# Performance work log

Hardware: AMD Instinct MI355X
Metric: run time of the kernel (lower is better)

Reference implementation:

```python
import jax, jax.numpy as jnp
import numpy as np

OUT, IN, R = 4096, 4096, 64
B, S = 4, 4096


def setup_inputs() -> dict:
    key = jax.random.key(0)
    ks = jax.random.split(key, 12)
    return {
        "x": jax.random.normal(ks[0], (B, S, IN), dtype=jnp.float32),
        "W": jax.random.normal(ks[1], (OUT, IN), dtype=jnp.float32) * 0.02,
        "bias": jax.random.normal(ks[2], (OUT,), dtype=jnp.float32) * 0.02,
        "U_top": jax.random.normal(ks[3], (OUT, R), dtype=jnp.float32) / np.sqrt(OUT),
        "S_top": jax.random.uniform(ks[4], (R,), dtype=jnp.float32),
        "Vh_top": jax.random.normal(ks[5], (R, IN), dtype=jnp.float32) / np.sqrt(IN),
        "U_tail": jax.random.normal(ks[6], (OUT, R), dtype=jnp.float32) / np.sqrt(OUT),
        "S_tail": jax.random.uniform(ks[7], (R,), dtype=jnp.float32),
        "Vh_tail": jax.random.normal(ks[8], (R, IN), dtype=jnp.float32) / np.sqrt(IN),
        "alpha": jax.random.normal(ks[9], (R,), dtype=jnp.float32) * 0.01,
        "beta": jax.random.normal(ks[10], (R,), dtype=jnp.float32) * 0.01,
        "R": jax.random.normal(ks[11], (R, R), dtype=jnp.float32) * 0.01,
    }


def reference(x, W, bias, U_top, S_top, Vh_top, U_tail, S_tail, Vh_tail, alpha, beta, R):
    # SALT top: gated singular-value correction, relu(S*alpha + beta)
    sigma_top = jax.nn.relu(S_top * alpha + beta)                    # [r]
    W_top_delta = (U_top * sigma_top[None, :]) @ Vh_top              # [out, in]
    # EDoRA tail: B R A with B = U_tail diag(S_tail), A = Vh_tail
    Bm = U_tail * S_tail[None, :]                                    # [out, r]
    delta_tail = Bm @ (R @ Vh_tail)                                  # [out, in]
    W_tilde = W + W_top_delta + delta_tail
    # F.linear: x @ W_tilde.T + bias
    return jnp.einsum('bsi,oi->bso', x, W_tilde) + bias
```

## Files before the change

kernel.cpp:

```cpp
#include <hip/hip_runtime.h>
#include <hip/hip_bf16.h>

#define OUT_DIM 4096
#define IN_DIM  4096
#define RANK    64
#define M_DIM   16384

typedef short  s16x8 __attribute__((ext_vector_type(8)));
typedef __bf16 b16x8 __attribute__((ext_vector_type(8)));
typedef float  f32x4 __attribute__((ext_vector_type(4)));

template <typename T>
__device__ static inline auto mfma_sel(T a, T b, f32x4 c, int)
    -> decltype(__builtin_amdgcn_mfma_f32_16x16x32_bf16(a, b, c, 0, 0, 0)) {
  return __builtin_amdgcn_mfma_f32_16x16x32_bf16(a, b, c, 0, 0, 0);
}
template <typename T>
__device__ static inline f32x4 mfma_sel(T a, T b, f32x4 c, long) {
  return __builtin_amdgcn_mfma_f32_16x16x32_bf16(
      __builtin_bit_cast(b16x8, a), __builtin_bit_cast(b16x8, b), c, 0, 0, 0);
}
__device__ static inline f32x4 mfma_bf16(s16x8 a, s16x8 b, f32x4 c) {
  return mfma_sel(a, b, c, 0);
}

__device__ static inline unsigned short f2bf(float f) {
  unsigned int u = __float_as_uint(f);
  u += 0x7fffu + ((u >> 16) & 1u);
  return (unsigned short)(u >> 16);
}

__device__ static inline void gload16(const unsigned short* g, unsigned short* l) {
  __builtin_amdgcn_global_load_lds(
      (const __attribute__((address_space(1))) void*)g,
      (__attribute__((address_space(3))) void*)l, 16, 0, 0);
}

__global__ void prep_kernel(const float* __restrict__ U_top, const float* __restrict__ S_top,
                            const float* __restrict__ alpha, const float* __restrict__ beta,
                            const float* __restrict__ U_tail, const float* __restrict__ S_tail,
                            float* __restrict__ A1, float* __restrict__ A2) {
  int idx = blockIdx.x * 256 + threadIdx.x;
  int r = idx & (RANK - 1);
  float sig = S_top[r] * alpha[r] + beta[r];
  sig = sig > 0.f ? sig : 0.f;
  A1[idx] = U_top[idx] * sig;
  A2[idx] = U_tail[idx] * S_tail[r];
}

__global__ void rv_kernel(const float* __restrict__ Rm, const float* __restrict__ Vh_tail,
                          float* __restrict__ RV) {
  const int i  = blockIdx.x * 256 + threadIdx.x;
  const int r0 = blockIdx.y * 8;
  float acc[8] = {};
  for (int q = 0; q < RANK; ++q) {
    float v = Vh_tail[(size_t)q * IN_DIM + i];
#pragma unroll
    for (int rr = 0; rr < 8; ++rr)
      acc[rr] = fmaf(Rm[(r0 + rr) * RANK + q], v, acc[rr]);
  }
#pragma unroll
  for (int rr = 0; rr < 8; ++rr) RV[(size_t)(r0 + rr) * IN_DIM + i] = acc[rr];
}

__global__ void cvt_kernel(const float* __restrict__ x, unsigned short* __restrict__ xb) {
  const long long n8 = (long long)M_DIM * IN_DIM / 8;
  long long idx = (long long)blockIdx.x * blockDim.x + threadIdx.x;
  const long long stride = (long long)gridDim.x * blockDim.x;
  for (; idx < n8; idx += stride) {
    const f32x4* p = (const f32x4*)(x + idx * 8);
    f32x4 v0 = p[0], v1 = p[1];
    s16x8 o;
    o[0] = (short)f2bf(v0[0]); o[1] = (short)f2bf(v0[1]);
    o[2] = (short)f2bf(v0[2]); o[3] = (short)f2bf(v0[3]);
    o[4] = (short)f2bf(v1[0]); o[5] = (short)f2bf(v1[1]);
    o[6] = (short)f2bf(v1[2]); o[7] = (short)f2bf(v1[3]);
    *(s16x8*)(xb + idx * 8) = o;
  }
}

#define WT_O 16
__global__ void wtilde_kernel(const float* __restrict__ W,  const float* __restrict__ A1,
                              const float* __restrict__ A2, const float* __restrict__ Vh_top,
                              const float* __restrict__ RV, unsigned short* __restrict__ Wb) {
  const int i  = blockIdx.x * 256 + threadIdx.x;
  const int o0 = blockIdx.y * WT_O;
  float acc[WT_O];
#pragma unroll
  for (int o = 0; o < WT_O; ++o) acc[o] = W[(size_t)(o0 + o) * IN_DIM + i];
#pragma unroll 4
  for (int r = 0; r < RANK; ++r) {
    float vt = Vh_top[(size_t)r * IN_DIM + i];
    float rv = RV[(size_t)r * IN_DIM + i];
#pragma unroll
    for (int o = 0; o < WT_O; ++o) {
      acc[o] = fmaf(A1[(o0 + o) * RANK + r], vt, acc[o]);
      acc[o] = fmaf(A2[(o0 + o) * RANK + r], rv, acc[o]);
    }
  }
#pragma unroll
  for (int o = 0; o < WT_O; ++o)
    Wb[(size_t)(o0 + o) * IN_DIM + i] = f2bf(acc[o]);
}

#define BM 256
#define BN 256
#define BK 64
#define NT (IN_DIM / BK)

__global__ __launch_bounds__(512, 2) void gemm_kernel(
    const unsigned short* __restrict__ A,
    const unsigned short* __restrict__ Bw,
    const float* __restrict__ bias,
    float* __restrict__ C) {
  __shared__ unsigned short lds[2][2][BM * BK];

  const int tid = threadIdx.x;
  const int l   = tid & 63;
  const int wid = tid >> 6;
  const int wr  = wid >> 2;
  const int wc  = wid & 3;

  const int bid = blockIdx.x;
  const int swz = (bid & 7) * 128 + (bid >> 3);
  const int nt_ = swz >> 6;
  const int mt_ = swz & 63;
  const long long tileM = (long long)mt_ * BM;
  const long long tileN = (long long)nt_ * BN;

  const int rbase = tid >> 3;
  const int c8    = (((tid & 7) ^ (rbase & 7)) << 3);
  const unsigned short* gA = A  + (tileM + rbase) * (long long)IN_DIM + c8;
  const unsigned short* gB = Bw + (tileN + rbase) * (long long)IN_DIM + c8;

  const int kgrp = l >> 4;
  const int x7   = l & 7;
  const int sc0  = (((0 * 4 + kgrp) ^ x7) << 3);
  const int sc1  = (((1 * 4 + kgrp) ^ x7) << 3);
  const int rba  = (wr * 128 + (l & 15)) * BK;
  const int rbb  = (wc * 64  + (l & 15)) * BK;

  f32x4 acc[8][4] = {};

  {
    unsigned short* la = &lds[0][0][tid * 8];
    unsigned short* lb = &lds[0][1][tid * 8];
#pragma unroll
    for (int j = 0; j < 4; ++j) {
      gload16(gA + (long long)j * 64 * IN_DIM, la + j * 4096);
      gload16(gB + (long long)j * 64 * IN_DIM, lb + j * 4096);
    }
    asm volatile("s_waitcnt vmcnt(0)" ::: "memory");
    asm volatile("s_barrier" ::: "memory");
  }

  int buf = 0;
  for (int t = 0; t < NT; ++t) {
    const long long ktn = (long long)(t + 1) * BK;
    const bool more = (t + 1 < NT);
    const unsigned short* lA = lds[buf][0];
    const unsigned short* lB = lds[buf][1];
    unsigned short* la1 = &lds[buf ^ 1][0][tid * 8];
    unsigned short* lb1 = &lds[buf ^ 1][1][tid * 8];

    s16x8 bfr[4][2];
#pragma unroll
    for (int q = 0; q < 4; ++q) {
      if (q == 0) {
#pragma unroll
        for (int n = 0; n < 4; ++n) {
          bfr[n][0] = *(const s16x8*)&lB[rbb + n * 16 * BK + sc0];
          bfr[n][1] = *(const s16x8*)&lB[rbb + n * 16 * BK + sc1];
        }
      }
      s16x8 afr[2][2];
#pragma unroll
      for (int m2 = 0; m2 < 2; ++m2) {
        afr[m2][0] = *(const s16x8*)&lA[rba + (q * 32 + m2 * 16) * BK + sc0];
        afr[m2][1] = *(const s16x8*)&lA[rba + (q * 32 + m2 * 16) * BK + sc1];
      }

      if (more) {
        if (q == 0) {
          gload16(gA + ktn, la1);
          gload16(gA + ktn + 2LL * 64 * IN_DIM, la1 + 2 * 4096);
        } else if (q == 1) {
          gload16(gA + ktn + 1LL * 64 * IN_DIM, la1 + 1 * 4096);
          gload16(gA + ktn + 3LL * 64 * IN_DIM, la1 + 3 * 4096);
        } else if (q == 2) {
          gload16(gB + ktn, lb1);
          gload16(gB + ktn + 1LL * 64 * IN_DIM, lb1 + 4096);
        } else {
          gload16(gB + ktn + 2LL * 64 * IN_DIM, lb1 + 2 * 4096);
          gload16(gB + ktn + 3LL * 64 * IN_DIM, lb1 + 3 * 4096);
        }
      }

      asm volatile("s_barrier" ::: "memory");

      __builtin_amdgcn_s_setprio(1);
#pragma unroll
      for (int m2 = 0; m2 < 2; ++m2)
#pragma unroll
        for (int n = 0; n < 4; ++n)
#pragma unroll
          for (int kk = 0; kk < 2; ++kk)
            acc[q * 2 + m2][n] = mfma_bf16(afr[m2][kk], bfr[n][kk], acc[q * 2 + m2][n]);
      __builtin_amdgcn_s_setprio(0);

      if (q == 3 && more) {
        asm volatile("s_waitcnt vmcnt(0)" ::: "memory");
      }
      asm volatile("s_barrier" ::: "memory");
    }
    buf ^= 1;
  }

  float bv[4];
#pragma unroll
  for (int n = 0; n < 4; ++n) bv[n] = bias[tileN + wc * 64 + n * 16 + (l & 15)];
#pragma unroll
  for (int m = 0; m < 8; ++m) {
    const long long rbase_c = tileM + wr * 128 + m * 16 + (l >> 4) * 4;
#pragma unroll
    for (int r = 0; r < 4; ++r) {
      float* crow = C + (size_t)(rbase_c + r) * OUT_DIM + tileN + wc * 64 + (l & 15);
#pragma unroll
      for (int n = 0; n < 4; ++n) crow[n * 16] = acc[m][n][r] + bv[n];
    }
  }
}

extern "C" void kernel_launch(void* const* d_in, const int* in_sizes, int n_in,
                              void* d_out, int out_size, void* d_ws, size_t ws_size,
                              hipStream_t stream) {
  const float* x       = (const float*)d_in[0];
  const float* W       = (const float*)d_in[1];
  const float* bias    = (const float*)d_in[2];
  const float* U_top   = (const float*)d_in[3];
  const float* S_top   = (const float*)d_in[4];
  const float* Vh_top  = (const float*)d_in[5];
  const float* U_tail  = (const float*)d_in[6];
  const float* S_tail  = (const float*)d_in[7];
  const float* Vh_tail = (const float*)d_in[8];
  const float* alpha   = (const float*)d_in[9];
  const float* beta    = (const float*)d_in[10];
  const float* Rm      = (const float*)d_in[11];

  char* ws = (char*)d_ws;
  unsigned short* xb = (unsigned short*)ws;
  unsigned short* Wb = (unsigned short*)(ws + (size_t)134217728);
  float* A1 = (float*)(ws + (size_t)134217728 + 33554432);
  float* A2 = A1 + (size_t)OUT_DIM * RANK;
  float* RV = A2 + (size_t)OUT_DIM * RANK;

  prep_kernel<<<(OUT_DIM * RANK) / 256, 256, 0, stream>>>(U_top, S_top, alpha, beta,
                                                          U_tail, S_tail, A1, A2);
  rv_kernel<<<dim3(IN_DIM / 256, RANK / 8), 256, 0, stream>>>(Rm, Vh_tail, RV);
  cvt_kernel<<<2048, 256, 0, stream>>>(x, xb);
  wtilde_kernel<<<dim3(IN_DIM / 256, OUT_DIM / WT_O), 256, 0, stream>>>(W, A1, A2,
                                                                        Vh_top, RV, Wb);
  gemm_kernel<<<(M_DIM / BM) * (OUT_DIM / BN), 512, 0, stream>>>(xb, Wb, bias,
                                                                 (float*)d_out);
}
```

Before: 761.1 us.

## Switch GEMM to 32x32x16 MFMA, relax load waits, fold prep kernel away

The main GEMM moves from 16x16x32 to 32x32x16 bf16 MFMA tiles. This reduces the number of LDS fragment reads and MFMA issues per tile and changes the accumulator and epilogue layout. The next-tile prefetch order is swapped to load B first. Partial vmcnt waits replace the full drain, so the wait on global-to-LDS loads overlaps more with compute. Separately, the prep kernel is removed by folding the sigma and S_tail scaling into the rv and wtilde kernels, which saves one launch and its intermediate buffers. The partial vmcnt counts must exactly match the outstanding loads, or the kernel could read stale LDS data.

```diff
diff --git a/kernel.cpp b/kernel.cpp
--- a/kernel.cpp
+++ b/kernel.cpp
@@ -6,22 +6,23 @@
 #define RANK    64
 #define M_DIM   16384
 
-typedef short  s16x8 __attribute__((ext_vector_type(8)));
-typedef __bf16 b16x8 __attribute__((ext_vector_type(8)));
-typedef float  f32x4 __attribute__((ext_vector_type(4)));
+typedef short  s16x8  __attribute__((ext_vector_type(8)));
+typedef __bf16 b16x8  __attribute__((ext_vector_type(8)));
+typedef float  f32x4  __attribute__((ext_vector_type(4)));
+typedef float  f32x16 __attribute__((ext_vector_type(16)));
 
 template <typename T>
-__device__ static inline auto mfma_sel(T a, T b, f32x4 c, int)
-    -> decltype(__builtin_amdgcn_mfma_f32_16x16x32_bf16(a, b, c, 0, 0, 0)) {
-  return __builtin_amdgcn_mfma_f32_16x16x32_bf16(a, b, c, 0, 0, 0);
+__device__ static inline auto mfma32_sel(T a, T b, f32x16 c, int)
+    -> decltype(__builtin_amdgcn_mfma_f32_32x32x16_bf16(a, b, c, 0, 0, 0)) {
+  return __builtin_amdgcn_mfma_f32_32x32x16_bf16(a, b, c, 0, 0, 0);
 }
 template <typename T>
-__device__ static inline f32x4 mfma_sel(T a, T b, f32x4 c, long) {
-  return __builtin_amdgcn_mfma_f32_16x16x32_bf16(
+__device__ static inline f32x16 mfma32_sel(T a, T b, f32x16 c, long) {
+  return __builtin_amdgcn_mfma_f32_32x32x16_bf16(
       __builtin_bit_cast(b16x8, a), __builtin_bit_cast(b16x8, b), c, 0, 0, 0);
 }
-__device__ static inline f32x4 mfma_bf16(s16x8 a, s16x8 b, f32x4 c) {
-  return mfma_sel(a, b, c, 0);
+__device__ static inline f32x16 mfma32(s16x8 a, s16x8 b, f32x16 c) {
+  return mfma32_sel(a, b, c, 0);
 }
 
 __device__ static inline unsigned short f2bf(float f) {
@@ -36,20 +37,8 @@
       (__attribute__((address_space(3))) void*)l, 16, 0, 0);
 }
 
-__global__ void prep_kernel(const float* __restrict__ U_top, const float* __restrict__ S_top,
-                            const float* __restrict__ alpha, const float* __restrict__ beta,
-                            const float* __restrict__ U_tail, const float* __restrict__ S_tail,
-                            float* __restrict__ A1, float* __restrict__ A2) {
-  int idx = blockIdx.x * 256 + threadIdx.x;
-  int r = idx & (RANK - 1);
-  float sig = S_top[r] * alpha[r] + beta[r];
-  sig = sig > 0.f ? sig : 0.f;
-  A1[idx] = U_top[idx] * sig;
-  A2[idx] = U_tail[idx] * S_tail[r];
-}
-
-__global__ void rv_kernel(const float* __restrict__ Rm, const float* __restrict__ Vh_tail,
-                          float* __restrict__ RV) {
+__global__ void rv2_kernel(const float* __restrict__ Rm, const float* __restrict__ Vh_tail,
+                           const float* __restrict__ S_tail, float* __restrict__ RV2) {
   const int i  = blockIdx.x * 256 + threadIdx.x;
   const int r0 = blockIdx.y * 8;
   float acc[8] = {};
@@ -60,7 +49,8 @@
       acc[rr] = fmaf(Rm[(r0 + rr) * RANK + q], v, acc[rr]);
   }
 #pragma unroll
-  for (int rr = 0; rr < 8; ++rr) RV[(size_t)(r0 + rr) * IN_DIM + i] = acc[rr];
+  for (int rr = 0; rr < 8; ++rr)
+    RV2[(size_t)(r0 + rr) * IN_DIM + i] = acc[rr] * S_tail[r0 + rr];
 }
 
 __global__ void cvt_kernel(const float* __restrict__ x, unsigned short* __restrict__ xb) {
@@ -80,9 +70,11 @@
 }
 
 #define WT_O 16
-__global__ void wtilde_kernel(const float* __restrict__ W,  const float* __restrict__ A1,
-                              const float* __restrict__ A2, const float* __restrict__ Vh_top,
-                              const float* __restrict__ RV, unsigned short* __restrict__ Wb) {
+__global__ void wtilde_kernel(const float* __restrict__ W,      const float* __restrict__ U_top,
+                              const float* __restrict__ S_top,  const float* __restrict__ alpha,
+                              const float* __restrict__ beta,   const float* __restrict__ U_tail,
+                              const float* __restrict__ Vh_top, const float* __restrict__ RV2,
+                              unsigned short* __restrict__ Wb) {
   const int i  = blockIdx.x * 256 + threadIdx.x;
   const int o0 = blockIdx.y * WT_O;
   float acc[WT_O];
@@ -90,12 +82,13 @@
   for (int o = 0; o < WT_O; ++o) acc[o] = W[(size_t)(o0 + o) * IN_DIM + i];
 #pragma unroll 4
   for (int r = 0; r < RANK; ++r) {
-    float vt = Vh_top[(size_t)r * IN_DIM + i];
-    float rv = RV[(size_t)r * IN_DIM + i];
+    float sig = fmaxf(fmaf(S_top[r], alpha[r], beta[r]), 0.f);
+    float vt  = Vh_top[(size_t)r * IN_DIM + i] * sig;
+    float rv  = RV2[(size_t)r * IN_DIM + i];
 #pragma unroll
     for (int o = 0; o < WT_O; ++o) {
-      acc[o] = fmaf(A1[(o0 + o) * RANK + r], vt, acc[o]);
-      acc[o] = fmaf(A2[(o0 + o) * RANK + r], rv, acc[o]);
+      acc[o] = fmaf(U_top[(o0 + o) * RANK + r],  vt, acc[o]);
+      acc[o] = fmaf(U_tail[(o0 + o) * RANK + r], rv, acc[o]);
     }
   }
 #pragma unroll
@@ -133,22 +126,23 @@
   const unsigned short* gA = A  + (tileM + rbase) * (long long)IN_DIM + c8;
   const unsigned short* gB = Bw + (tileN + rbase) * (long long)IN_DIM + c8;
 
-  const int kgrp = l >> 4;
-  const int x7   = l & 7;
-  const int sc0  = (((0 * 4 + kgrp) ^ x7) << 3);
-  const int sc1  = (((1 * 4 + kgrp) ^ x7) << 3);
-  const int rba  = (wr * 128 + (l & 15)) * BK;
-  const int rbb  = (wc * 64  + (l & 15)) * BK;
-
-  f32x4 acc[8][4] = {};
+  const int l31 = l & 31;
+  int sck[4];
+#pragma unroll
+  for (int kk = 0; kk < 4; ++kk)
+    sck[kk] = (((kk * 2 + (l >> 5)) ^ (l & 7)) << 3);
+  const int rbaA = (wr * 128 + l31) * BK;
+  const int rbaB = (wc * 64  + l31) * BK;
+
+  f32x16 acc[4][2] = {};
 
   {
     unsigned short* la = &lds[0][0][tid * 8];
     unsigned short* lb = &lds[0][1][tid * 8];
 #pragma unroll
     for (int j = 0; j < 4; ++j) {
+      gload16(gB + (long long)j * 64 * IN_DIM, lb + j * 4096);
       gload16(gA + (long long)j * 64 * IN_DIM, la + j * 4096);
-      gload16(gB + (long long)j * 64 * IN_DIM, lb + j * 4096);
     }
     asm volatile("s_waitcnt vmcnt(0)" ::: "memory");
     asm volatile("s_barrier" ::: "memory");
@@ -163,36 +157,34 @@
     unsigned short* la1 = &lds[buf ^ 1][0][tid * 8];
     unsigned short* lb1 = &lds[buf ^ 1][1][tid * 8];
 
-    s16x8 bfr[4][2];
+    s16x8 bfr[2][4];
 #pragma unroll
     for (int q = 0; q < 4; ++q) {
       if (q == 0) {
 #pragma unroll
-        for (int n = 0; n < 4; ++n) {
-          bfr[n][0] = *(const s16x8*)&lB[rbb + n * 16 * BK + sc0];
-          bfr[n][1] = *(const s16x8*)&lB[rbb + n * 16 * BK + sc1];
-        }
-      }
-      s16x8 afr[2][2];
-#pragma unroll
-      for (int m2 = 0; m2 < 2; ++m2) {
-        afr[m2][0] = *(const s16x8*)&lA[rba + (q * 32 + m2 * 16) * BK + sc0];
-        afr[m2][1] = *(const s16x8*)&lA[rba + (q * 32 + m2 * 16) * BK + sc1];
-      }
+        for (int n = 0; n < 2; ++n)
+#pragma unroll
+          for (int kk = 0; kk < 4; ++kk)
+            bfr[n][kk] = *(const s16x8*)&lB[rbaB + n * 32 * BK + sck[kk]];
+      }
+      s16x8 afr[4];
+#pragma unroll
+      for (int kk = 0; kk < 4; ++kk)
+        afr[kk] = *(const s16x8*)&lA[rbaA + q * 32 * BK + sck[kk]];
 
       if (more) {
         if (q == 0) {
+          gload16(gB + ktn, lb1);
+          gload16(gB + ktn + 1LL * 64 * IN_DIM, lb1 + 4096);
+        } else if (q == 1) {
+          gload16(gB + ktn + 2LL * 64 * IN_DIM, lb1 + 2 * 4096);
+          gload16(gB + ktn + 3LL * 64 * IN_DIM, lb1 + 3 * 4096);
+        } else if (q == 2) {
           gload16(gA + ktn, la1);
           gload16(gA + ktn + 2LL * 64 * IN_DIM, la1 + 2 * 4096);
-        } else if (q == 1) {
+        } else {
           gload16(gA + ktn + 1LL * 64 * IN_DIM, la1 + 1 * 4096);
           gload16(gA + ktn + 3LL * 64 * IN_DIM, la1 + 3 * 4096);
-        } else if (q == 2) {
-          gload16(gB + ktn, lb1);
-          gload16(gB + ktn + 1LL * 64 * IN_DIM, lb1 + 4096);
-        } else {
-          gload16(gB + ktn + 2LL * 64 * IN_DIM, lb1 + 2 * 4096);
-          gload16(gB + ktn + 3LL * 64 * IN_DIM, lb1 + 3 * 4096);
         }
       }
 
@@ -200,33 +192,36 @@
 
       __builtin_amdgcn_s_setprio(1);
 #pragma unroll
-      for (int m2 = 0; m2 < 2; ++m2)
-#pragma unroll
-        for (int n = 0; n < 4; ++n)
-#pragma unroll
-          for (int kk = 0; kk < 2; ++kk)
-            acc[q * 2 + m2][n] = mfma_bf16(afr[m2][kk], bfr[n][kk], acc[q * 2 + m2][n]);
+      for (int kk = 0; kk < 4; ++kk)
+#pragma unroll
+        for (int n = 0; n < 2; ++n)
+          acc[q][n] = mfma32(afr[kk], bfr[n][kk], acc[q][n]);
       __builtin_amdgcn_s_setprio(0);
 
+      if (q == 1) {
+        if (more) asm volatile("s_waitcnt vmcnt(4)" ::: "memory");
+        else      asm volatile("s_waitcnt vmcnt(0)" ::: "memory");
+      }
       if (q == 3 && more) {
-        asm volatile("s_waitcnt vmcnt(0)" ::: "memory");
+        asm volatile("s_waitcnt vmcnt(2)" ::: "memory");
       }
       asm volatile("s_barrier" ::: "memory");
     }
     buf ^= 1;
   }
 
-  float bv[4];
-#pragma unroll
-  for (int n = 0; n < 4; ++n) bv[n] = bias[tileN + wc * 64 + n * 16 + (l & 15)];
-#pragma unroll
-  for (int m = 0; m < 8; ++m) {
-    const long long rbase_c = tileM + wr * 128 + m * 16 + (l >> 4) * 4;
-#pragma unroll
-    for (int r = 0; r < 4; ++r) {
-      float* crow = C + (size_t)(rbase_c + r) * OUT_DIM + tileN + wc * 64 + (l & 15);
-#pragma unroll
-      for (int n = 0; n < 4; ++n) crow[n * 16] = acc[m][n][r] + bv[n];
+  float bv[2];
+#pragma unroll
+  for (int n = 0; n < 2; ++n) bv[n] = bias[tileN + wc * 64 + n * 32 + l31];
+#pragma unroll
+  for (int m = 0; m < 4; ++m) {
+    const long long rowm = tileM + wr * 128 + m * 32 + 4 * (l >> 5);
+#pragma unroll
+    for (int r = 0; r < 16; ++r) {
+      const long long row = rowm + (r & 3) + 8 * (r >> 2);
+      float* crow = C + (size_t)row * OUT_DIM + tileN + wc * 64 + l31;
+#pragma unroll
+      for (int n = 0; n < 2; ++n) crow[n * 32] = acc[m][n][r] + bv[n];
     }
   }
 }
@@ -248,18 +243,14 @@
   const float* Rm      = (const float*)d_in[11];
 
   char* ws = (char*)d_ws;
-  unsigned short* xb = (unsigned short*)ws;
-  unsigned short* Wb = (unsigned short*)(ws + (size_t)134217728);
-  float* A1 = (float*)(ws + (size_t)134217728 + 33554432);
-  float* A2 = A1 + (size_t)OUT_DIM * RANK;
-  float* RV = A2 + (size_t)OUT_DIM * RANK;
-
-  prep_kernel<<<(OUT_DIM * RANK) / 256, 256, 0, stream>>>(U_top, S_top, alpha, beta,
-                                                          U_tail, S_tail, A1, A2);
-  rv_kernel<<<dim3(IN_DIM / 256, RANK / 8), 256, 0, stream>>>(Rm, Vh_tail, RV);
+  unsigned short* xb  = (unsigned short*)ws;
+  unsigned short* Wb  = (unsigned short*)(ws + (size_t)134217728);
+  float*          RV2 = (float*)(ws + (size_t)134217728 + 33554432);
+
+  rv2_kernel<<<dim3(IN_DIM / 256, RANK / 8), 256, 0, stream>>>(Rm, Vh_tail, S_tail, RV2);
   cvt_kernel<<<2048, 256, 0, stream>>>(x, xb);
-  wtilde_kernel<<<dim3(IN_DIM / 256, OUT_DIM / WT_O), 256, 0, stream>>>(W, A1, A2,
-                                                                        Vh_top, RV, Wb);
+  wtilde_kernel<<<dim3(IN_DIM / 256, OUT_DIM / WT_O), 256, 0, stream>>>(
+      W, U_top, S_top, alpha, beta, U_tail, Vh_top, RV2, Wb);
   gemm_kernel<<<(M_DIM / BM) * (OUT_DIM / BN), 512, 0, stream>>>(xb, Wb, bias,
                                                                  (float*)d_out);
 }
```

Result: no change. 752.8 us (-1.1%).
